# Performance work log

Measured on AMD Instinct MI355X. Metric: run time of the kernel, lower is better.

The kernel has to match this reference:

```python
import jax, jax.numpy as jnp
import numpy as np

INPUT_DIM = 1024
EMBED_DIM = 1024
NUM_HEADS = 16
HEAD_DIM = EMBED_DIM // NUM_HEADS


def _xavier_uniform(key, shape):
    fan_in, fan_out = shape[1], shape[0]
    limit = float(np.sqrt(6.0 / (fan_in + fan_out)))
    return jax.random.uniform(key, shape, jnp.float32, -limit, limit)


def setup_inputs() -> dict:
    key = jax.random.key(0)
    kx, kqkv, ko = jax.random.split(key, 3)
    x = jax.random.normal(kx, (2, 2048, INPUT_DIM), jnp.float32)
    # torch Linear stores weight as [out, in]; we keep that convention
    w_qkv = _xavier_uniform(kqkv, (3 * EMBED_DIM, INPUT_DIM))
    b_qkv = jnp.zeros((3 * EMBED_DIM,), jnp.float32)
    w_o = _xavier_uniform(ko, (EMBED_DIM, EMBED_DIM))
    b_o = jnp.zeros((EMBED_DIM,), jnp.float32)
    return {"x": x, "w_qkv": w_qkv, "b_qkv": b_qkv, "w_o": w_o, "b_o": b_o}


def reference(x, w_qkv, b_qkv, w_o, b_o):
    B, S, _ = x.shape
    H, D = NUM_HEADS, HEAD_DIM
    qkv = jnp.einsum("bsi,oi->bso", x, w_qkv) + b_qkv          # [B,S,3E]
    qkv = qkv.reshape(B, S, H, 3 * D).transpose(0, 2, 1, 3)    # [B,H,S,3D]
    q, k, v = jnp.split(qkv, 3, axis=-1)                        # each [B,H,S,D]
    scores = jnp.einsum("bhqd,bhkd->bhqk", q, k) / jnp.sqrt(jnp.float32(D))
    attn = jax.nn.softmax(scores, axis=-1)                      # [B,H,S,S]
    vals = jnp.einsum("bhqk,bhkd->bhqd", attn, v)               # [B,H,S,D]
    vals = vals.transpose(0, 2, 1, 3).reshape(B, S, H * D)      # [B,S,E]
    return jnp.einsum("bse,oe->bso", vals, w_o) + b_o
```

## Files before the change

kernel.cpp:

```cpp
#include <hip/hip_runtime.h>
#include <hip/hip_bf16.h>


typedef __attribute__((ext_vector_type(8))) short bf16x8;
typedef __attribute__((ext_vector_type(4))) short bf16x4;
typedef __attribute__((ext_vector_type(4))) float f32x4;

#define MFMA16(a, b, c) __builtin_amdgcn_mfma_f32_16x16x32_bf16((a), (b), (c), 0, 0, 0)

#if __has_builtin(__builtin_amdgcn_exp2f)
#define EXP2F(x) __builtin_amdgcn_exp2f(x)
#else
#define EXP2F(x) exp2f(x)
#endif

static __device__ __forceinline__ unsigned short f2bf_bits(float v) {
    __hip_bfloat16 h = __float2bfloat16(v);
    return *reinterpret_cast<unsigned short*>(&h);
}

static __device__ __forceinline__ bf16x8 cvt8(const float* p) {
    const f32x4 a = reinterpret_cast<const f32x4*>(p)[0];
    const f32x4 b = reinterpret_cast<const f32x4*>(p)[1];
    bf16x8 r;
    r[0] = (short)f2bf_bits(a[0]); r[1] = (short)f2bf_bits(a[1]);
    r[2] = (short)f2bf_bits(a[2]); r[3] = (short)f2bf_bits(a[3]);
    r[4] = (short)f2bf_bits(b[0]); r[5] = (short)f2bf_bits(b[1]);
    r[6] = (short)f2bf_bits(b[2]); r[7] = (short)f2bf_bits(b[3]);
    return r;
}

__device__ __forceinline__ bf16x8 ldg8(const __hip_bfloat16* p) {
    return *reinterpret_cast<const bf16x8*>(p);
}

__device__ __forceinline__ void load16_lds(const __hip_bfloat16* g, unsigned short* l) {
    __builtin_amdgcn_global_load_lds(
        (const __attribute__((address_space(1))) void*)g,
        (__attribute__((address_space(3))) void*)l, 16, 0, 0);
}

__global__ __launch_bounds__(256)
void cast2_f32_bf16(const float* __restrict__ x, __hip_bfloat16* __restrict__ xb,
                    const float* __restrict__ w, __hip_bfloat16* __restrict__ wb) {
    const int bid = blockIdx.x;
    const float* src = (bid < 512) ? x : w;
    __hip_bfloat16* dst = (bid < 512) ? xb : wb;
    const int rb = (bid < 512) ? bid : (bid - 512);
    const size_t base = (size_t)rb * 8192 + (size_t)threadIdx.x * 32;
#pragma unroll
    for (int i = 0; i < 4; ++i)
        *reinterpret_cast<bf16x8*>(dst + base + i * 8) = cvt8(src + base + i * 8);
}

__global__ __launch_bounds__(256)
void cast_f32_bf16(const float* __restrict__ src, __hip_bfloat16* __restrict__ dst) {
    const size_t base = ((size_t)blockIdx.x * 256 + threadIdx.x) * 32;
#pragma unroll
    for (int i = 0; i < 4; ++i)
        *reinterpret_cast<bf16x8*>(dst + base + i * 8) = cvt8(src + base + i * 8);
}

__global__ __launch_bounds__(256)
void qkv_gemm(const __hip_bfloat16* __restrict__ xb,
              const __hip_bfloat16* __restrict__ wb,
              const float* __restrict__ bqkv,
              __hip_bfloat16* __restrict__ Q,
              __hip_bfloat16* __restrict__ K,
              __hip_bfloat16* __restrict__ Vt) {
    __shared__ unsigned short As[2][128 * 32];
    __shared__ unsigned short Bs[2][128 * 32];

    const int tid  = threadIdx.x;
    const int lane = tid & 63;
    const int wv   = tid >> 6;
    const int quad = lane >> 4;
    const int l16  = lane & 15;
    const int wm   = wv >> 1;
    const int wn   = wv & 1;

    const int bid = blockIdx.x;
    const int xcd = bid & 7;
    const int r   = bid >> 3;
    const int m0  = (r / 3) * 128;
    const int n0  = (xcd * 3 + (r % 3)) * 128;

    const __hip_bfloat16* agl = xb + (size_t)(m0 + wv * 32 + (lane >> 2)) * 1024 + (lane & 3) * 8;
    const __hip_bfloat16* bgl = wb + (size_t)(n0 + wv * 32 + (lane >> 2)) * 1024 + (lane & 3) * 8;

    f32x4 zv = {0.f, 0.f, 0.f, 0.f};
    f32x4 acc[4][4];
#pragma unroll
    for (int ii = 0; ii < 4; ++ii)
#pragma unroll
        for (int jj = 0; jj < 4; ++jj) acc[ii][jj] = zv;

    load16_lds(agl, &As[0][(wv * 32) * 32]);
    load16_lds(agl + 16 * 1024, &As[0][(wv * 32 + 16) * 32]);
    load16_lds(bgl, &Bs[0][(wv * 32) * 32]);
    load16_lds(bgl + 16 * 1024, &Bs[0][(wv * 32 + 16) * 32]);
    __syncthreads();

    for (int k0 = 0; k0 < 1024; k0 += 32) {
        const int p = (k0 >> 5) & 1;
        if (k0 + 32 < 1024) {
            const int q = p ^ 1;
            load16_lds(agl + k0 + 32, &As[q][(wv * 32) * 32]);
            load16_lds(agl + 16 * 1024 + k0 + 32, &As[q][(wv * 32 + 16) * 32]);
            load16_lds(bgl + k0 + 32, &Bs[q][(wv * 32) * 32]);
            load16_lds(bgl + 16 * 1024 + k0 + 32, &Bs[q][(wv * 32 + 16) * 32]);
        }
        bf16x8 af[4], bf[4];
#pragma unroll
        for (int ii = 0; ii < 4; ++ii)
            af[ii] = *reinterpret_cast<const bf16x8*>(
                &As[p][(wm * 64 + ii * 16 + l16) * 32 + quad * 8]);
#pragma unroll
        for (int jj = 0; jj < 4; ++jj)
            bf[jj] = *reinterpret_cast<const bf16x8*>(
                &Bs[p][(wn * 64 + jj * 16 + l16) * 32 + quad * 8]);
#pragma unroll
        for (int ii = 0; ii < 4; ++ii)
#pragma unroll
            for (int jj = 0; jj < 4; ++jj)
                acc[ii][jj] = MFMA16(af[ii], bf[jj], acc[ii][jj]);
        __syncthreads();
    }

    const float QSCALE = 0.18033688011f;

#pragma unroll
    for (int jj = 0; jj < 4; ++jj) {
        const int n = n0 + wn * 64 + jj * 16 + l16;
        const float bias = bqkv[n];
        const int h = n / 192;
        const int r2 = n - h * 192;
        const int t = r2 >> 6;
        const int d = r2 & 63;
#pragma unroll
        for (int ii = 0; ii < 4; ++ii) {
            const int mb = m0 + wm * 64 + ii * 16 + quad * 4;
            const int b = mb >> 11;
            const int s0 = mb & 2047;
            const int bh = b * 16 + h;
            if (t == 2) {
                bf16x4 pk;
#pragma unroll
                for (int i = 0; i < 4; ++i)
                    pk[i] = (short)f2bf_bits(acc[ii][jj][i] + bias);
                *reinterpret_cast<bf16x4*>(&Vt[((size_t)bh * 64 + d) * 2048 + s0]) = pk;
            } else {
#pragma unroll
                for (int i = 0; i < 4; ++i) {
                    const float v = acc[ii][jj][i] + bias;
                    if (t == 0)
                        Q[((size_t)bh * 2048 + s0 + i) * 64 + d] = __float2bfloat16(v * QSCALE);
                    else
                        K[((size_t)bh * 2048 + s0 + i) * 64 + d] = __float2bfloat16(v);
                }
            }
        }
    }
}

__global__ __launch_bounds__(512, 4)
void attn_kernel(const __hip_bfloat16* __restrict__ Q,
                 const __hip_bfloat16* __restrict__ K,
                 const __hip_bfloat16* __restrict__ Vt,
                 __hip_bfloat16* __restrict__ AO) {
    __shared__ unsigned short Ks0[2][32 * 40];
    __shared__ unsigned short Ks1[2][32 * 40];
    __shared__ unsigned short Vs[2][64 * 40];

    const int tid  = threadIdx.x;
    const int lane = tid & 63;
    const int wv   = tid >> 6;
    const int quad = lane >> 4;
    const int l16  = lane & 15;

    const int blk = blockIdx.x;
    const int xcd = blk & 7;
    const int sub = blk >> 3;
    const int bh  = xcd * 4 + (sub & 3);
    const int qb  = sub >> 2;
    const int q0  = qb * 128 + wv * 16;
    const int b   = bh >> 4;
    const int h   = bh & 15;

    const __hip_bfloat16* Qp = Q  + (size_t)bh * 131072;
    const __hip_bfloat16* Kp = K  + (size_t)bh * 131072;
    const __hip_bfloat16* Vp = Vt + (size_t)bh * 131072;

    bf16x8 bQ[2];
#pragma unroll
    for (int dh = 0; dh < 2; ++dh)
        bQ[dh] = ldg8(Qp + (size_t)(q0 + l16) * 64 + dh * 32 + quad * 8);

    unsigned short* s0;
    unsigned short* s1;
    const __hip_bfloat16* sgp;
    size_t sstep;
    if (wv < 4) {
        const int half   = wv >> 1;
        const int rowblk = wv & 1;
        const int krow   = rowblk * 16 + l16;
        const int keyg   = (l16 >> 2) * 8 + rowblk * 4 + (l16 & 3);
        sgp   = Kp + (size_t)keyg * 64 + half * 32 + quad * 8;
        unsigned short* base0 = half ? &Ks1[0][0] : &Ks0[0][0];
        unsigned short* base1 = half ? &Ks1[1][0] : &Ks0[1][0];
        s0 = base0 + krow * 40 + quad * 8;
        s1 = base1 + krow * 40 + quad * 8;
        sstep = 32 * 64;
    } else {
        const int vrow = (wv - 4) * 16 + l16;
        sgp   = Vp + (size_t)vrow * 2048 + quad * 8;
        s0 = &Vs[0][vrow * 40 + quad * 8];
        s1 = &Vs[1][vrow * 40 + quad * 8];
        sstep = 32;
    }

    f32x4 zv = {0.f, 0.f, 0.f, 0.f};
    f32x4 Of[4];
#pragma unroll
    for (int jj = 0; jj < 4; ++jj) Of[jj] = zv;
    float li = 0.f;

    bf16x8 g = ldg8(sgp);
    *reinterpret_cast<bf16x8*>(s0) = g;
    g = ldg8(sgp + sstep);
    __syncthreads();

    for (int kt = 0; kt < 64; ++kt) {
        const int p = kt & 1;
        if (kt < 63)
            *reinterpret_cast<bf16x8*>(p ? s0 : s1) = g;
        if (kt < 62)
            g = ldg8(sgp + (size_t)(kt + 2) * sstep);

        const bf16x8 aKA0 = *reinterpret_cast<const bf16x8*>(&Ks0[p][l16 * 40 + quad * 8]);
        const bf16x8 aKA1 = *reinterpret_cast<const bf16x8*>(&Ks1[p][l16 * 40 + quad * 8]);
        const bf16x8 aKB0 = *reinterpret_cast<const bf16x8*>(&Ks0[p][(16 + l16) * 40 + quad * 8]);
        const bf16x8 aKB1 = *reinterpret_cast<const bf16x8*>(&Ks1[p][(16 + l16) * 40 + quad * 8]);
        bf16x8 aV[4];
#pragma unroll
        for (int jj = 0; jj < 4; ++jj)
            aV[jj] = *reinterpret_cast<const bf16x8*>(&Vs[p][(jj * 16 + l16) * 40 + quad * 8]);

        f32x4 sA = zv, sB = zv;
        sA = MFMA16(aKA0, bQ[0], sA);
        sA = MFMA16(aKA1, bQ[1], sA);
        sB = MFMA16(aKB0, bQ[0], sB);
        sB = MFMA16(aKB1, bQ[1], sB);

        float pA[4], pB[4];
#pragma unroll
        for (int i = 0; i < 4; ++i) {
            pA[i] = EXP2F(sA[i]);
            pB[i] = EXP2F(sB[i]);
        }
        li += ((pA[0] + pA[1]) + (pA[2] + pA[3]))
            + ((pB[0] + pB[1]) + (pB[2] + pB[3]));

        bf16x8 bP;
        bP[0] = (short)f2bf_bits(pA[0]); bP[1] = (short)f2bf_bits(pA[1]);
        bP[2] = (short)f2bf_bits(pA[2]); bP[3] = (short)f2bf_bits(pA[3]);
        bP[4] = (short)f2bf_bits(pB[0]); bP[5] = (short)f2bf_bits(pB[1]);
        bP[6] = (short)f2bf_bits(pB[2]); bP[7] = (short)f2bf_bits(pB[3]);

#pragma unroll
        for (int jj = 0; jj < 4; ++jj)
            Of[jj] = MFMA16(aV[jj], bP, Of[jj]);

        __syncthreads();
    }

    li += __shfl_xor(li, 16);
    li += __shfl_xor(li, 32);

    {
        const float linv = 1.f / li;
        const int s = q0 + l16;
        __hip_bfloat16* aop = AO + (((size_t)b * 2048 + s) * 16 + h) * 64;
#pragma unroll
        for (int jj = 0; jj < 4; ++jj) {
            bf16x4 pk;
#pragma unroll
            for (int i = 0; i < 4; ++i)
                pk[i] = (short)f2bf_bits(Of[jj][i] * linv);
            *reinterpret_cast<bf16x4*>(aop + jj * 16 + quad * 4) = pk;
        }
    }
}

__global__ __launch_bounds__(256)
void out_gemm(const __hip_bfloat16* __restrict__ A,
              const __hip_bfloat16* __restrict__ wob,
              const float* __restrict__ bo,
              float* __restrict__ out) {
    __shared__ unsigned short As[2][64 * 32];
    __shared__ unsigned short Bs[2][128 * 32];

    const int tid  = threadIdx.x;
    const int lane = tid & 63;
    const int wv   = tid >> 6;
    const int quad = lane >> 4;
    const int l16  = lane & 15;
    const int wm   = wv >> 1;
    const int wn   = wv & 1;

    const int bid = blockIdx.x;
    const int m0  = (bid >> 3) * 64;
    const int n0  = (bid & 7) * 128;

    const __hip_bfloat16* agl = A   + (size_t)(m0 + wv * 16 + (lane >> 2)) * 1024 + (lane & 3) * 8;
    const __hip_bfloat16* bgl = wob + (size_t)(n0 + wv * 32 + (lane >> 2)) * 1024 + (lane & 3) * 8;

    f32x4 zv = {0.f, 0.f, 0.f, 0.f};
    f32x4 acc[2][4];
#pragma unroll
    for (int ii = 0; ii < 2; ++ii)
#pragma unroll
        for (int jj = 0; jj < 4; ++jj) acc[ii][jj] = zv;

    load16_lds(agl, &As[0][(wv * 16) * 32]);
    load16_lds(bgl, &Bs[0][(wv * 32) * 32]);
    load16_lds(bgl + 16 * 1024, &Bs[0][(wv * 32 + 16) * 32]);
    __syncthreads();

    for (int k0 = 0; k0 < 1024; k0 += 32) {
        const int p = (k0 >> 5) & 1;
        if (k0 + 32 < 1024) {
            const int q = p ^ 1;
            load16_lds(agl + k0 + 32, &As[q][(wv * 16) * 32]);
            load16_lds(bgl + k0 + 32, &Bs[q][(wv * 32) * 32]);
            load16_lds(bgl + 16 * 1024 + k0 + 32, &Bs[q][(wv * 32 + 16) * 32]);
        }
        bf16x8 af[2], bf[4];
#pragma unroll
        for (int ii = 0; ii < 2; ++ii)
            af[ii] = *reinterpret_cast<const bf16x8*>(
                &As[p][(wm * 32 + ii * 16 + l16) * 32 + quad * 8]);
#pragma unroll
        for (int jj = 0; jj < 4; ++jj)
            bf[jj] = *reinterpret_cast<const bf16x8*>(
                &Bs[p][(wn * 64 + jj * 16 + l16) * 32 + quad * 8]);
#pragma unroll
        for (int ii = 0; ii < 2; ++ii)
#pragma unroll
            for (int jj = 0; jj < 4; ++jj)
                acc[ii][jj] = MFMA16(af[ii], bf[jj], acc[ii][jj]);
        __syncthreads();
    }

#pragma unroll
    for (int jj = 0; jj < 4; ++jj) {
        const int n = n0 + wn * 64 + jj * 16 + l16;
        const float bias = bo[n];
#pragma unroll
        for (int ii = 0; ii < 2; ++ii) {
#pragma unroll
            for (int i = 0; i < 4; ++i) {
                const int m = m0 + wm * 32 + ii * 16 + quad * 4 + i;
                out[(size_t)m * 1024 + n] = acc[ii][jj][i] + bias;
            }
        }
    }
}

extern "C" void kernel_launch(void* const* d_in, const int* in_sizes, int n_in,
                              void* d_out, int out_size, void* d_ws, size_t ws_size,
                              hipStream_t stream) {
    const float* x    = (const float*)d_in[0];
    const float* wqkv = (const float*)d_in[1];
    const float* bqkv = (const float*)d_in[2];
    const float* wo   = (const float*)d_in[3];
    const float* bo   = (const float*)d_in[4];
    float* out = (float*)d_out;

    __hip_bfloat16* ws = (__hip_bfloat16*)d_ws;
    __hip_bfloat16* Q   = ws;
    __hip_bfloat16* K   = ws + (size_t)4194304;
    __hip_bfloat16* Vt  = ws + (size_t)8388608;
    __hip_bfloat16* AO  = ws + (size_t)12582912;
    __hip_bfloat16* wob = Q;

    __hip_bfloat16* xb     = (__hip_bfloat16*)d_out;
    __hip_bfloat16* wqkvb  = xb + (size_t)4194304;

    cast2_f32_bf16<<<dim3(896), 256, 0, stream>>>(x, xb, wqkv, wqkvb);
    qkv_gemm<<<dim3(768), 256, 0, stream>>>(xb, wqkvb, bqkv, Q, K, Vt);
    attn_kernel<<<dim3(512), 512, 0, stream>>>(Q, K, Vt, AO);
    cast_f32_bf16<<<dim3(128), 256, 0, stream>>>(wo, wob);
    out_gemm<<<dim3(512), 256, 0, stream>>>(AO, wob, bo, out);
}
```

Measured before the change: 196.7 us.

## Load K/V fragments directly from global into registers, dropping LDS staging

The attention kernel no longer stages K and V tiles through shared memory with per-iteration barriers. Each wave now loads its own K and V MFMA fragments straight from global memory into registers, double-buffered across two key tiles. Blocks shrink to 256 threads (4 waves, 64 queries) and the grid doubles to 1024. This removes LDS traffic and __syncthreads, at the cost of every wave re-reading the same K/V data from global/L2 and holding more fragment registers.

```diff
diff --git a/kernel.cpp b/kernel.cpp
--- a/kernel.cpp
+++ b/kernel.cpp
@@ -163,15 +163,11 @@
     }
 }
 
-__global__ __launch_bounds__(512, 4)
+__global__ __launch_bounds__(256, 4)
 void attn_kernel(const __hip_bfloat16* __restrict__ Q,
                  const __hip_bfloat16* __restrict__ K,
                  const __hip_bfloat16* __restrict__ Vt,
                  __hip_bfloat16* __restrict__ AO) {
-    __shared__ unsigned short Ks0[2][32 * 40];
-    __shared__ unsigned short Ks1[2][32 * 40];
-    __shared__ unsigned short Vs[2][64 * 40];
-
     const int tid  = threadIdx.x;
     const int lane = tid & 63;
     const int wv   = tid >> 6;
@@ -183,7 +179,7 @@
     const int sub = blk >> 3;
     const int bh  = xcd * 4 + (sub & 3);
     const int qb  = sub >> 2;
-    const int q0  = qb * 128 + wv * 16;
+    const int q0  = qb * 64 + wv * 16;
     const int b   = bh >> 4;
     const int h   = bh & 15;
 
@@ -191,66 +187,39 @@
     const __hip_bfloat16* Kp = K  + (size_t)bh * 131072;
     const __hip_bfloat16* Vp = Vt + (size_t)bh * 131072;
 
-    bf16x8 bQ[2];
-#pragma unroll
-    for (int dh = 0; dh < 2; ++dh)
-        bQ[dh] = ldg8(Qp + (size_t)(q0 + l16) * 64 + dh * 32 + quad * 8);
-
-    unsigned short* s0;
-    unsigned short* s1;
-    const __hip_bfloat16* sgp;
-    size_t sstep;
-    if (wv < 4) {
-        const int half   = wv >> 1;
-        const int rowblk = wv & 1;
-        const int krow   = rowblk * 16 + l16;
-        const int keyg   = (l16 >> 2) * 8 + rowblk * 4 + (l16 & 3);
-        sgp   = Kp + (size_t)keyg * 64 + half * 32 + quad * 8;
-        unsigned short* base0 = half ? &Ks1[0][0] : &Ks0[0][0];
-        unsigned short* base1 = half ? &Ks1[1][0] : &Ks0[1][0];
-        s0 = base0 + krow * 40 + quad * 8;
-        s1 = base1 + krow * 40 + quad * 8;
-        sstep = 32 * 64;
-    } else {
-        const int vrow = (wv - 4) * 16 + l16;
-        sgp   = Vp + (size_t)vrow * 2048 + quad * 8;
-        s0 = &Vs[0][vrow * 40 + quad * 8];
-        s1 = &Vs[1][vrow * 40 + quad * 8];
-        sstep = 32;
-    }
-
-    f32x4 zv = {0.f, 0.f, 0.f, 0.f};
-    f32x4 Of[4];
-#pragma unroll
-    for (int jj = 0; jj < 4; ++jj) Of[jj] = zv;
+    const bf16x8 bQ0 = ldg8(Qp + (size_t)(q0 + l16) * 64 + quad * 8);
+    const bf16x8 bQ1 = ldg8(Qp + (size_t)(q0 + l16) * 64 + 32 + quad * 8);
+
+    const int key_a = (l16 >> 2) * 8 + (l16 & 3);
+    const __hip_bfloat16* ka = Kp + (size_t)key_a * 64 + quad * 8;
+    const __hip_bfloat16* kb = ka + 4 * 64;
+    const __hip_bfloat16* va = Vp + (size_t)l16 * 2048 + quad * 8;
+
+    const f32x4 zv = {0.f, 0.f, 0.f, 0.f};
+    f32x4 Of0 = zv, Of1 = zv, Of2 = zv, Of3 = zv;
     float li = 0.f;
 
-    bf16x8 g = ldg8(sgp);
-    *reinterpret_cast<bf16x8*>(s0) = g;
-    g = ldg8(sgp + sstep);
-    __syncthreads();
-
-    for (int kt = 0; kt < 64; ++kt) {
-        const int p = kt & 1;
-        if (kt < 63)
-            *reinterpret_cast<bf16x8*>(p ? s0 : s1) = g;
-        if (kt < 62)
-            g = ldg8(sgp + (size_t)(kt + 2) * sstep);
-
-        const bf16x8 aKA0 = *reinterpret_cast<const bf16x8*>(&Ks0[p][l16 * 40 + quad * 8]);
-        const bf16x8 aKA1 = *reinterpret_cast<const bf16x8*>(&Ks1[p][l16 * 40 + quad * 8]);
-        const bf16x8 aKB0 = *reinterpret_cast<const bf16x8*>(&Ks0[p][(16 + l16) * 40 + quad * 8]);
-        const bf16x8 aKB1 = *reinterpret_cast<const bf16x8*>(&Ks1[p][(16 + l16) * 40 + quad * 8]);
-        bf16x8 aV[4];
-#pragma unroll
-        for (int jj = 0; jj < 4; ++jj)
-            aV[jj] = *reinterpret_cast<const bf16x8*>(&Vs[p][(jj * 16 + l16) * 40 + quad * 8]);
-
+    struct Frags { bf16x8 kA0, kA1, kB0, kB1, v0, v1, v2, v3; };
+
+    auto LOAD = [&](int kt, Frags& F) {
+        const size_t ko = (size_t)kt * 2048;
+        const size_t vo = (size_t)kt * 32;
+        F.kA0 = ldg8(ka + ko);
+        F.kA1 = ldg8(ka + ko + 32);
+        F.kB0 = ldg8(kb + ko);
+        F.kB1 = ldg8(kb + ko + 32);
+        F.v0  = ldg8(va + vo);
+        F.v1  = ldg8(va + vo + (size_t)16 * 2048);
+        F.v2  = ldg8(va + vo + (size_t)32 * 2048);
+        F.v3  = ldg8(va + vo + (size_t)48 * 2048);
+    };
+
+    auto COMPUTE = [&](const Frags& F) {
         f32x4 sA = zv, sB = zv;
-        sA = MFMA16(aKA0, bQ[0], sA);
-        sA = MFMA16(aKA1, bQ[1], sA);
-        sB = MFMA16(aKB0, bQ[0], sB);
-        sB = MFMA16(aKB1, bQ[1], sB);
+        sA = MFMA16(F.kA0, bQ0, sA);
+        sA = MFMA16(F.kA1, bQ1, sA);
+        sB = MFMA16(F.kB0, bQ0, sB);
+        sB = MFMA16(F.kB1, bQ1, sB);
 
         float pA[4], pB[4];
 #pragma unroll
@@ -267,11 +236,19 @@
         bP[4] = (short)f2bf_bits(pB[0]); bP[5] = (short)f2bf_bits(pB[1]);
         bP[6] = (short)f2bf_bits(pB[2]); bP[7] = (short)f2bf_bits(pB[3]);
 
-#pragma unroll
-        for (int jj = 0; jj < 4; ++jj)
-            Of[jj] = MFMA16(aV[jj], bP, Of[jj]);
-
-        __syncthreads();
+        Of0 = MFMA16(F.v0, bP, Of0);
+        Of1 = MFMA16(F.v1, bP, Of1);
+        Of2 = MFMA16(F.v2, bP, Of2);
+        Of3 = MFMA16(F.v3, bP, Of3);
+    };
+
+    Frags fa, fb;
+    LOAD(0, fa);
+    for (int kt = 0; kt < 64; kt += 2) {
+        LOAD(kt + 1, fb);
+        COMPUTE(fa);
+        if (kt + 2 < 64) LOAD(kt + 2, fa);
+        COMPUTE(fb);
     }
 
     li += __shfl_xor(li, 16);
@@ -281,6 +258,7 @@
         const float linv = 1.f / li;
         const int s = q0 + l16;
         __hip_bfloat16* aop = AO + (((size_t)b * 2048 + s) * 16 + h) * 64;
+        f32x4 Of[4] = {Of0, Of1, Of2, Of3};
 #pragma unroll
         for (int jj = 0; jj < 4; ++jj) {
             bf16x4 pk;
@@ -389,7 +367,7 @@
 
     cast2_f32_bf16<<<dim3(896), 256, 0, stream>>>(x, xb, wqkv, wqkvb);
     qkv_gemm<<<dim3(768), 256, 0, stream>>>(xb, wqkvb, bqkv, Q, K, Vt);
-    attn_kernel<<<dim3(512), 512, 0, stream>>>(Q, K, Vt, AO);
+    attn_kernel<<<dim3(1024), 256, 0, stream>>>(Q, K, Vt, AO);
     cast_f32_bf16<<<dim3(128), 256, 0, stream>>>(wo, wob);
     out_gemm<<<dim3(512), 256, 0, stream>>>(AO, wob, bo, out);
 }
```

New measurement: 375.6 us. +90.9%, slower.
